# Performance work log

Measured on AMD Instinct MI355X. Metric: run time of the kernel, lower is better.

Reference implementation:

```python
import jax, jax.numpy as jnp
import numpy as np

EMBED_DIM = 1024
NUM_HEADS = 8
HEAD_DIM = EMBED_DIM // NUM_HEADS
SEQ_LEN = 128              # T: leaf sequence length of the tree
NODE_LEN = 2 * SEQ_LEN - 1 # Tk: nodes of a binary tree over T leaves
BATCH = 4
TGT_LEN = 128


def _tree_spans(lo, hi, out):
    # spans (lo, hi) of a balanced binary constituency tree, lo <= hi
    out.append((lo, hi))
    if lo == hi:
        return
    mid = (lo + hi) // 2
    _tree_spans(lo, mid, out)
    _tree_spans(mid + 1, hi, out)


def setup_inputs() -> dict:
    key = jax.random.key(0)
    ks = jax.random.split(key, 6)
    query = jax.random.normal(ks[0], (TGT_LEN, BATCH, EMBED_DIM), jnp.float32)
    key_t = jax.random.normal(ks[1], (NODE_LEN, BATCH, EMBED_DIM), jnp.float32)
    value = jax.random.normal(ks[2], (NODE_LEN, BATCH, EMBED_DIM), jnp.float32)
    spans = []
    _tree_spans(0, SEQ_LEN - 1, spans)
    spans = np.asarray(spans, dtype=np.int64)            # [Tk, 2], row <= col
    indices = jnp.asarray(np.broadcast_to(spans[None], (BATCH, NODE_LEN, 2)).copy())
    s = 1.0 / np.sqrt(EMBED_DIM)  # xavier-ish scale
    in_proj_weight = jax.random.uniform(ks[3], (3 * EMBED_DIM, EMBED_DIM), jnp.float32, -s, s)
    in_proj_bias = jnp.zeros((3 * EMBED_DIM,), jnp.float32)
    out_proj_weight = jax.random.uniform(ks[4], (EMBED_DIM, EMBED_DIM), jnp.float32, -s, s)
    out_proj_bias = jnp.zeros((EMBED_DIM,), jnp.float32)
    return {"query": query, "key": key_t, "value": value, "indices": indices,
            "in_proj_weight": in_proj_weight, "in_proj_bias": in_proj_bias,
            "out_proj_weight": out_proj_weight, "out_proj_bias": out_proj_bias}


def _forward(query, key, value, indices, in_proj_weight, in_proj_bias,
             out_proj_weight, out_proj_bias):
    T, H, D = SEQ_LEN, NUM_HEADS, HEAD_DIM
    lq, B, E = query.shape
    Tk = key.shape[0]
    wq, wk, wv = jnp.split(in_proj_weight, 3, axis=0)
    bq, bk, bv = jnp.split(in_proj_bias, 3)
    q = (query @ wq.T + bq) * (D ** -0.5)   # scaling = head_dim ** -0.5
    k = key @ wk.T + bk
    v = value @ wv.T + bv

    def to_heads(x):  # [L, B, E] -> [B*H, L, D]
        L = x.shape[0]
        return x.reshape(L, B * H, D).transpose(1, 0, 2)

    q, k, v = to_heads(q), to_heads(k), to_heads(v)

    # indices2flat_indices: fl_idx = row * T + col  -> [B, Tk]
    fl_idx = indices[:, :, 0] * T + indices[:, :, 1]

    # seq2matrix: scatter node keys into [B, H, D, T*T] span matrix
    k_b = k.reshape(B, H, Tk, D)

    def scat(kb, fb):  # kb [H, Tk, D], fb [Tk]
        return jnp.zeros((H, D, T * T), kb.dtype).at[:, :, fb].set(kb.transpose(0, 2, 1))

    mat_k = jax.vmap(scat)(k_b, fl_idx).reshape(B * H, D, T, T)

    # query2matrix + dot product: affinity[b,q,r,c] = <q_bq, k_node(r,c)> * triu(r<=c)
    triu = jnp.triu(jnp.ones((T, T), q.dtype))
    aff = jnp.einsum('bqd,bdrc->bqrc', q, mat_k) * triu  # [B*H, lq, T, T]

    # DP (hierarchical) accumulation over contained spans:
    # acc[r,c] = sum_{r <= r' <= c' <= c} aff[r',c']
    acc = jnp.flip(jnp.cumsum(jnp.flip(aff, axis=2), axis=2), axis=2)
    acc = jnp.cumsum(acc, axis=3)

    # gather scores back at node span positions -> [B, H, lq, Tk]
    acc = acc.reshape(B, H, lq, T * T)
    scores = jnp.take_along_axis(acc, fl_idx[:, None, None, :], axis=3)

    w = jax.nn.softmax(scores.reshape(B * H, lq, Tk), axis=-1)
    attn = jnp.einsum('bqn,bnd->bqd', w, v)              # [B*H, lq, D]
    attn = attn.transpose(1, 0, 2).reshape(lq, B, E)
    return attn @ out_proj_weight.T + out_proj_bias


def reference(query, key, value, indices, in_proj_weight, in_proj_bias,
              out_proj_weight, out_proj_bias):
    return _forward(query, key, value, indices, in_proj_weight, in_proj_bias,
                    out_proj_weight, out_proj_bias)
```

## Files before the change

### kernel.cpp

```cpp
#include <hip/hip_runtime.h>
#include <math.h>

#define EMBED 1024
#define NHEAD 8
#define HDIM 128
#define TK 255
#define BATCH 4
#define LQ 128
#define BH 32

typedef __attribute__((ext_vector_type(4))) float f32x4;
typedef __attribute__((ext_vector_type(8))) short short8;
typedef __attribute__((ext_vector_type(4))) short short4v;

static __device__ __forceinline__ unsigned short f2bf(float f) {
    unsigned u = __float_as_uint(f);
    u += 0x7FFFu + ((u >> 16) & 1u);
    return (unsigned short)(u >> 16);
}
static __device__ __forceinline__ float bfbits2f(unsigned short s) {
    return __uint_as_float(((unsigned)s) << 16);
}

__global__ __launch_bounds__(256) void prep_kernel(
    const float* __restrict__ query, const float* __restrict__ key_t,
    const float* __restrict__ value, const float* __restrict__ ipw,
    const float* __restrict__ opw,
    unsigned short* __restrict__ apk, unsigned short* __restrict__ wpk)
{
    const int blk = blockIdx.x;
    const int t = threadIdx.x;
    if (blk < 128) {
        const int b = blk >> 5, eg = blk & 31;
        const int cl = t & 31, seg = t >> 5;
        const int e = eg * 32 + cl;
        __shared__ float tot[8][33];
        float vals[32];
        float acc = 0.f;
        const int nhi = seg * 32 + 31;
        #pragma unroll
        for (int i = 0; i < 32; ++i) {
            const int n = nhi - i;
            float v = 0.f;
            if (n < TK) v = key_t[(long)(n * 4 + b) * 1024 + e];
            acc += v;
            vals[i] = acc;
        }
        tot[seg][cl] = acc;
        __syncthreads();
        float add = 0.f;
        #pragma unroll
        for (int s = 0; s < 8; ++s) if (s > seg) add += tot[s][cl];
        #pragma unroll
        for (int i = 0; i < 32; ++i) {
            const int n = nhi - i;
            const float f = vals[i] + add;
            const unsigned short hv = f2bf(f);
            const unsigned short lv = f2bf(f - bfbits2f(hv));
            unsigned short* dst = apk + (long)(512 + b * 256 + n) * 2048 + e;
            dst[0] = hv;
            dst[1024] = lv;
        }
    } else {
        const int APKC = 1536 * 256;
        const int TOT = APKC + 4096 * 256;
        for (int idx = (blk - 128) * 256 + t; idx < TOT; idx += 2048 * 256) {
            const bool isA = idx < APKC;
            const int rel = isA ? idx : idx - APKC;
            const int row = rel >> 8, c4 = rel & 255;
            const float* src = nullptr; long srow = 0;
            unsigned short* dst;
            bool wlo = true;
            if (isA) {
                if (row < 512) { src = query; srow = row; dst = apk + (long)row * 2048; }
                else {
                    const int vr = row - 512;
                    dst = apk + (long)(1536 + vr) * 2048;
                    if (vr < 1020) { src = value; srow = vr; }
                }
            } else {
                dst = wpk + (long)row * 2048;
                if (row < 3072) { src = ipw; srow = row; }
                else { src = opw; srow = row - 3072; }
                wlo = (row < 2048);
            }
            float4 f = make_float4(0.f, 0.f, 0.f, 0.f);
            if (src) f = *(const float4*)(src + srow * 1024 + c4 * 4);
            const unsigned short h0 = f2bf(f.x), h1 = f2bf(f.y), h2 = f2bf(f.z), h3 = f2bf(f.w);
            short4v hv;
            hv[0] = (short)h0; hv[1] = (short)h1; hv[2] = (short)h2; hv[3] = (short)h3;
            *(short4v*)(dst + c4 * 4) = hv;
            if (wlo) {
                short4v lv;
                lv[0] = (short)f2bf(f.x - bfbits2f(h0));
                lv[1] = (short)f2bf(f.y - bfbits2f(h1));
                lv[2] = (short)f2bf(f.z - bfbits2f(h2));
                lv[3] = (short)f2bf(f.w - bfbits2f(h3));
                *(short4v*)(dst + 1024 + c4 * 4) = lv;
            }
        }
    }
}

template<int BM, int BN, int TERMS, int EPI>
__device__ __forceinline__ void bgemm2(
    const unsigned short* __restrict__ A,
    const unsigned short* __restrict__ B,
    const float* __restrict__ bias,
    void* __restrict__ Cv, long ldc, float scale,
    int m0, int n0, unsigned char* lds)
{
    constexpr int AH = 0;
    constexpr int AL = BM * 128;
    constexpr int BHo = 2 * BM * 128;
    constexpr int BLo = BHo + BN * 128;
    constexpr int FM2 = BM / 32, FN2 = BN / 32;
    constexpr int CA = BM / 32;
    constexpr int CB = BN / 32;
    const int t = threadIdx.x, lane = t & 63, wave = t >> 6;
    const int wm = wave >> 1, wn = wave & 1;

    f32x4 acc[FM2][FN2];
    #pragma unroll
    for (int i = 0; i < FM2; ++i)
        #pragma unroll
        for (int j = 0; j < FN2; ++j)
            #pragma unroll
            for (int e = 0; e < 4; ++e) acc[i][j][e] = 0.f;

    const int srow_a = t >> 3, su = t & 7;
    short8 rah[CA], ral[CA], rbh[CB], rbl[CB];

    #pragma unroll
    for (int c = 0; c < CA; ++c) {
        const long base = (long)(m0 + c * 32 + srow_a) * 2048 + su * 8;
        rah[c] = *(const short8*)(A + base);
        ral[c] = *(const short8*)(A + base + 1024);
    }
    #pragma unroll
    for (int c = 0; c < CB; ++c) {
        const long base = (long)(n0 + c * 32 + srow_a) * 2048 + su * 8;
        rbh[c] = *(const short8*)(B + base);
        if (TERMS == 3) rbl[c] = *(const short8*)(B + base + 1024);
    }

    for (int kt = 0; kt < 16; ++kt) {
        #pragma unroll
        for (int c = 0; c < CA; ++c) {
            const int row = c * 32 + srow_a;
            const int byte = row * 128 + ((su ^ (row & 7)) << 4);
            *(short8*)(lds + AH + byte) = rah[c];
            *(short8*)(lds + AL + byte) = ral[c];
        }
        #pragma unroll
        for (int c = 0; c < CB; ++c) {
            const int row = c * 32 + srow_a;
            const int byte = row * 128 + ((su ^ (row & 7)) << 4);
            *(short8*)(lds + BHo + byte) = rbh[c];
            if (TERMS == 3) *(short8*)(lds + BLo + byte) = rbl[c];
        }
        __syncthreads();
        if (kt + 1 < 16) {
            const int off = (kt + 1) * 64;
            #pragma unroll
            for (int c = 0; c < CA; ++c) {
                const long base = (long)(m0 + c * 32 + srow_a) * 2048 + off + su * 8;
                rah[c] = *(const short8*)(A + base);
                ral[c] = *(const short8*)(A + base + 1024);
            }
            #pragma unroll
            for (int c = 0; c < CB; ++c) {
                const long base = (long)(n0 + c * 32 + srow_a) * 2048 + off + su * 8;
                rbh[c] = *(const short8*)(B + base);
                if (TERMS == 3) rbl[c] = *(const short8*)(B + base + 1024);
            }
        }
        #pragma unroll
        for (int ks = 0; ks < 2; ++ks) {
            short8 afh[FM2], afl[FM2], bgh[FN2], bgl[FN2];
            #pragma unroll
            for (int fm = 0; fm < FM2; ++fm) {
                const int row = wm * (BM / 2) + fm * 16 + (lane & 15);
                const int byte = row * 128 + (((ks * 4 + (lane >> 4)) ^ (row & 7)) << 4);
                afh[fm] = *(const short8*)(lds + AH + byte);
                afl[fm] = *(const short8*)(lds + AL + byte);
            }
            #pragma unroll
            for (int fn = 0; fn < FN2; ++fn) {
                const int row = wn * (BN / 2) + fn * 16 + (lane & 15);
                const int byte = row * 128 + (((ks * 4 + (lane >> 4)) ^ (row & 7)) << 4);
                bgh[fn] = *(const short8*)(lds + BHo + byte);
                if (TERMS == 3) bgl[fn] = *(const short8*)(lds + BLo + byte);
            }
            #pragma unroll
            for (int fm = 0; fm < FM2; ++fm)
                #pragma unroll
                for (int fn = 0; fn < FN2; ++fn) {
                    acc[fm][fn] = __builtin_amdgcn_mfma_f32_16x16x32_bf16(afh[fm], bgh[fn], acc[fm][fn], 0, 0, 0);
                    acc[fm][fn] = __builtin_amdgcn_mfma_f32_16x16x32_bf16(afl[fm], bgh[fn], acc[fm][fn], 0, 0, 0);
                    if (TERMS == 3)
                        acc[fm][fn] = __builtin_amdgcn_mfma_f32_16x16x32_bf16(afh[fm], bgl[fn], acc[fm][fn], 0, 0, 0);
                }
        }
        __syncthreads();
    }

    #pragma unroll
    for (int fm = 0; fm < FM2; ++fm)
        #pragma unroll
        for (int i = 0; i < 4; ++i) {
            const int m = m0 + wm * (BM / 2) + fm * 16 + ((lane >> 4) << 2) + i;
            #pragma unroll
            for (int fn = 0; fn < FN2; ++fn) {
                const int n = n0 + wn * (BN / 2) + fn * 16 + (lane & 15);
                float v = acc[fm][fn][i];
                if (EPI == 0) {
                    float* C = (float*)Cv;
                    if (bias) v += bias[n];
                    C[(long)m * ldc + n] = v * scale;
                } else if (EPI == 1) {
                    float* C = (float*)Cv;
                    v += (float)(255 - (m & 255)) * bias[n];
                    C[(long)m * ldc + n] = v;
                } else if (EPI == 2) {
                    unsigned short* C = (unsigned short*)Cv;
                    const float val = (v + bias[n]) * scale;
                    const unsigned short hv = f2bf(val);
                    const unsigned short lv = f2bf(val - bfbits2f(hv));
                    C[(long)m * 2048 + n] = hv;
                    C[(long)m * 2048 + 1024 + n] = lv;
                } else {
                    unsigned short* C = (unsigned short*)Cv;
                    const float val = v + bias[n];
                    C[(long)m * 1024 + n] = f2bf(val);
                }
            }
        }
}

__global__ __launch_bounds__(256) void qkvb_kernel(
    const unsigned short* __restrict__ apk, const unsigned short* __restrict__ wpk,
    const float* __restrict__ ipb,
    unsigned short* __restrict__ qpk, float* __restrict__ sbuf,
    unsigned short* __restrict__ vpk, float qscale)
{
    __shared__ __align__(16) unsigned char lds[4 * 64 * 128];
    const int lid = blockIdx.y * 16 + blockIdx.x;
    const int xcd = lid & 7, slot = lid >> 3;
    const int y = xcd * 5 + (slot >> 4);
    const int x = slot & 15;
    if (y < 8) {
        bgemm2<64, 64, 3, 2>(apk, wpk, ipb, qpk, 2048, qscale,
                             y * 64, x * 64, lds);
    } else if (y < 24) {
        bgemm2<64, 64, 3, 1>(apk + 512L * 2048, wpk + 1024L * 2048, ipb + 1024, sbuf, 1024, 1.f,
                             (y - 8) * 64, x * 64, lds);
    } else {
        bgemm2<64, 64, 2, 3>(apk + 1536L * 2048, wpk + 2048L * 2048, ipb + 2048, vpk, 1024, 1.f,
                             (y - 24) * 64, x * 64, lds);
    }
}

__global__ __launch_bounds__(256) void outprojb_kernel(
    const unsigned short* __restrict__ apk2, const unsigned short* __restrict__ wpk,
    const float* __restrict__ opb, float* __restrict__ out)
{
    __shared__ __align__(16) unsigned char lds[(2 * 32 + 64) * 128];
    const int lid = blockIdx.x;
    const int xcd = lid & 7, slot = lid >> 3;
    const int y = xcd * 2 + (slot >> 4);
    const int x = slot & 15;
    bgemm2<32, 64, 2, 0>(apk2, wpk + 3072L * 2048, opb, out, 1024, 1.f,
                         y * 32, x * 64, lds);
}

#define F_QH 0
#define F_QL 8192
#define F_KH 16384
#define F_KL 32768
#define F_PH 49152
#define F_RED 65536
#define F_INV 66048

__global__ __launch_bounds__(256, 2) void fused_attn_kernel(
    const unsigned short* __restrict__ qpk, const float* __restrict__ sbuf,
    const unsigned short* __restrict__ vpk, const int* __restrict__ indices,
    unsigned short* __restrict__ apk2)
{
    __shared__ __align__(16) unsigned char lds[66176];
    __shared__ int onode[256];
    const int lid = blockIdx.x;
    const int xcd = lid & 7, slot = lid >> 3;
    const int bh = xcd * 4 + (slot >> 2), qq = slot & 3;
    const int b = bh >> 3, h = bh & 7;
    const int t = threadIdx.x, lane = t & 63, wave = t >> 6;
    const int wm = wave >> 1, wn = wave & 1;
    float* red = (float*)(lds + F_RED);
    float* inv = (float*)(lds + F_INV);

    if (t < TK) {
        const int r0 = indices[(b * TK + t) * 2 + 0];
        const int c0 = indices[(b * TK + t) * 2 + 1];
        onode[t] = t + 2 * (c0 - r0) + 1;
    } else if (t < 256) {
        onode[t] = 255;
    }

    {
        #pragma unroll
        for (int rr = 0; rr < 4; ++rr) {
            const int chunk = rr * 256 + t;
            const int row = chunk >> 5;
            const int rem = chunk & 31;
            const int plane = rem >> 4, u = rem & 15;
            const int tq = qq * 32 + row;
            short8 v = *(const short8*)(qpk + (long)(tq * 4 + b) * 2048 + plane * 1024 + h * 128 + u * 8);
            const int byte = row * 256 + ((u ^ (row & 15)) << 4);
            *(short8*)(lds + (plane ? F_QL : F_QH) + byte) = v;
        }
    }

    f32x4 acc[4][2];
    #pragma unroll
    for (int nb = 0; nb < 4; ++nb)
        #pragma unroll
        for (int j = 0; j < 2; ++j)
            #pragma unroll
            for (int e = 0; e < 4; ++e) acc[nb][j][e] = 0.f;

    #pragma unroll
    for (int nb = 0; nb < 4; ++nb) {
        __syncthreads();
        {
            const int c4 = t & 31, r8 = t >> 5;
            const float* sb = sbuf + (long)b * 256 * 1024 + h * 128 + c4 * 4;
            #pragma unroll
            for (int rr = 0; rr < 8; ++rr) {
                const int nl = r8 + rr * 8;
                const int node = nb * 64 + nl;
                float4 f0 = *(const float4*)(sb + (long)node * 1024);
                float4 f1 = *(const float4*)(sb + (long)onode[node] * 1024);
                float4 f = make_float4(f0.x - f1.x, f0.y - f1.y, f0.z - f1.z, f0.w - f1.w);
                const unsigned short h0 = f2bf(f.x), h1 = f2bf(f.y), h2 = f2bf(f.z), h3 = f2bf(f.w);
                short4v hv, lv;
                hv[0] = (short)h0; hv[1] = (short)h1; hv[2] = (short)h2; hv[3] = (short)h3;
                lv[0] = (short)f2bf(f.x - bfbits2f(h0));
                lv[1] = (short)f2bf(f.y - bfbits2f(h1));
                lv[2] = (short)f2bf(f.z - bfbits2f(h2));
                lv[3] = (short)f2bf(f.w - bfbits2f(h3));
                const int byte = nl * 256 + ((((c4 >> 1) ^ (nl & 15)) << 4) | ((c4 & 1) << 3));
                *(short4v*)(lds + F_KH + byte) = hv;
                *(short4v*)(lds + F_KL + byte) = lv;
            }
        }
        __syncthreads();
        #pragma unroll
        for (int ks = 0; ks < 4; ++ks) {
            short8 ah, al, bh_[2], bl[2];
            {
                const int row = wm * 16 + (lane & 15);
                const int byte = row * 256 + (((ks * 4 + (lane >> 4)) ^ (row & 15)) << 4);
                ah = *(const short8*)(lds + F_QH + byte);
                al = *(const short8*)(lds + F_QL + byte);
            }
            #pragma unroll
            for (int fn = 0; fn < 2; ++fn) {
                const int row = wn * 32 + fn * 16 + (lane & 15);
                const int byte = row * 256 + (((ks * 4 + (lane >> 4)) ^ (row & 15)) << 4);
                bh_[fn] = *(const short8*)(lds + F_KH + byte);
                bl[fn] = *(const short8*)(lds + F_KL + byte);
            }
            #pragma unroll
            for (int fn = 0; fn < 2; ++fn) {
                acc[nb][fn] = __builtin_amdgcn_mfma_f32_16x16x32_bf16(ah, bh_[fn], acc[nb][fn], 0, 0, 0);
                acc[nb][fn] = __builtin_amdgcn_mfma_f32_16x16x32_bf16(al, bh_[fn], acc[nb][fn], 0, 0, 0);
                acc[nb][fn] = __builtin_amdgcn_mfma_f32_16x16x32_bf16(ah, bl[fn], acc[nb][fn], 0, 0, 0);
            }
        }
    }

    float pmax[4] = {-1e30f, -1e30f, -1e30f, -1e30f};
    #pragma unroll
    for (int nb = 0; nb < 4; ++nb)
        #pragma unroll
        for (int fn = 0; fn < 2; ++fn)
            #pragma unroll
            for (int i = 0; i < 4; ++i) {
                const int col = nb * 64 + wn * 32 + fn * 16 + (lane & 15);
                const float s = (col < TK) ? acc[nb][fn][i] : -1e30f;
                pmax[i] = fmaxf(pmax[i], s);
            }
    #pragma unroll
    for (int off = 1; off < 16; off <<= 1)
        #pragma unroll
        for (int i = 0; i < 4; ++i) pmax[i] = fmaxf(pmax[i], __shfl_xor(pmax[i], off));
    if ((lane & 15) == 0) {
        #pragma unroll
        for (int i = 0; i < 4; ++i) {
            const int row = wm * 16 + ((lane >> 4) << 2) + i;
            red[wn * 32 + row] = pmax[i];
        }
    }
    __syncthreads();
    float rm[4];
    #pragma unroll
    for (int i = 0; i < 4; ++i) {
        const int row = wm * 16 + ((lane >> 4) << 2) + i;
        rm[i] = fmaxf(red[row], red[32 + row]);
    }
    float psum[4] = {0.f, 0.f, 0.f, 0.f};
    #pragma unroll
    for (int nb = 0; nb < 4; ++nb)
        #pragma unroll
        for (int fn = 0; fn < 2; ++fn)
            #pragma unroll
            for (int i = 0; i < 4; ++i) {
                const int col = nb * 64 + wn * 32 + fn * 16 + (lane & 15);
                const int row = wm * 16 + ((lane >> 4) << 2) + i;
                float p = 0.f;
                if (col < TK) p = __expf(acc[nb][fn][i] - rm[i]);
                psum[i] += p;
                const unsigned short hp = f2bf(p);
                const int u = ((col >> 3) ^ ((row & 15) << 1));
                const int byte = row * 512 + (u << 4) + (col & 7) * 2;
                *(unsigned short*)(lds + F_PH + byte) = hp;
            }
    #pragma unroll
    for (int off = 1; off < 16; off <<= 1)
        #pragma unroll
        for (int i = 0; i < 4; ++i) psum[i] += __shfl_xor(psum[i], off);
    if ((lane & 15) == 0) {
        #pragma unroll
        for (int i = 0; i < 4; ++i) {
            const int row = wm * 16 + ((lane >> 4) << 2) + i;
            red[64 + wn * 32 + row] = psum[i];
        }
    }
    __syncthreads();
    if (wn == 0 && (lane & 15) == 0) {
        #pragma unroll
        for (int i = 0; i < 4; ++i) {
            const int row = wm * 16 + ((lane >> 4) << 2) + i;
            inv[row] = 1.f / (red[64 + row] + red[96 + row]);
        }
    }

    f32x4 accO[4];
    #pragma unroll
    for (int fn = 0; fn < 4; ++fn)
        #pragma unroll
        for (int e = 0; e < 4; ++e) accO[fn][e] = 0.f;

    #pragma unroll
    for (int nb = 0; nb < 4; ++nb) {
        __syncthreads();
        {
            const int c8 = t & 15, r16 = t >> 4;
            #pragma unroll
            for (int rr = 0; rr < 4; ++rr) {
                const int nl = r16 + rr * 16;
                const int node = nb * 64 + nl;
                short8 v = {0, 0, 0, 0, 0, 0, 0, 0};
                if (node < TK) v = *(const short8*)(vpk + (long)(node * 4 + b) * 1024 + h * 128 + c8 * 8);
                #pragma unroll
                for (int j = 0; j < 8; ++j) {
                    const int d = c8 * 8 + j;
                    const int byte = d * 128 + ((((nl >> 3) ^ (d & 7)) << 4) | ((nl & 7) << 1));
                    *(unsigned short*)(lds + F_KH + byte) = (unsigned short)v[j];
                }
            }
        }
        __syncthreads();
        #pragma unroll
        for (int ks = 0; ks < 2; ++ks) {
            short8 pa, vb[4];
            {
                const int row = wm * 16 + (lane & 15);
                const int u = (nb * 8 + ks * 4 + (lane >> 4)) ^ ((row & 15) << 1);
                const int byte = row * 512 + (u << 4);
                pa = *(const short8*)(lds + F_PH + byte);
            }
            #pragma unroll
            for (int fn = 0; fn < 4; ++fn) {
                const int d = wn * 64 + fn * 16 + (lane & 15);
                const int u = (ks * 4 + (lane >> 4)) ^ (d & 7);
                const int byte = d * 128 + (u << 4);
                vb[fn] = *(const short8*)(lds + F_KH + byte);
            }
            #pragma unroll
            for (int fn = 0; fn < 4; ++fn)
                accO[fn] = __builtin_amdgcn_mfma_f32_16x16x32_bf16(pa, vb[fn], accO[fn], 0, 0, 0);
        }
    }

    __syncthreads();
    #pragma unroll
    for (int i = 0; i < 4; ++i) {
        const int row = wm * 16 + ((lane >> 4) << 2) + i;
        const float iv = inv[row];
        const int arow = (qq * 32 + row) * 4 + b;
        #pragma unroll
        for (int fn = 0; fn < 4; ++fn) {
            const int col = h * 128 + wn * 64 + fn * 16 + (lane & 15);
            const float val = accO[fn][i] * iv;
            const unsigned short hv = f2bf(val);
            const unsigned short lv = f2bf(val - bfbits2f(hv));
            apk2[(long)arow * 2048 + col] = hv;
            apk2[(long)arow * 2048 + 1024 + col] = lv;
        }
    }
}

extern "C" void kernel_launch(void* const* d_in, const int* in_sizes, int n_in,
                              void* d_out, int out_size, void* d_ws, size_t ws_size,
                              hipStream_t stream) {
    const float* query   = (const float*)d_in[0];
    const float* key_t   = (const float*)d_in[1];
    const float* value   = (const float*)d_in[2];
    const int*   indices = (const int*)d_in[3];
    const float* ipw     = (const float*)d_in[4];
    const float* ipb     = (const float*)d_in[5];
    const float* opw     = (const float*)d_in[6];
    const float* opb     = (const float*)d_in[7];
    float* out = (float*)d_out;

    float* ws = (float*)d_ws;
    float* sbuf = ws;
    unsigned short* qpk = (unsigned short*)(sbuf + 1048576);
    unsigned short* vpk = qpk + 512L * 2048;
    unsigned short* apk = vpk + 1024L * 1024;
    unsigned short* wpk = apk + 2560L * 2048;
    unsigned short* apk2 = apk;

    const float qscale = 0.08838834764831843f;

    prep_kernel<<<dim3(2176), 256, 0, stream>>>(query, key_t, value, ipw, opw, apk, wpk);

    qkvb_kernel<<<dim3(16, 40), 256, 0, stream>>>(apk, wpk, ipb, qpk, sbuf, vpk, qscale);

    fused_attn_kernel<<<dim3(128), 256, 0, stream>>>(qpk, sbuf, vpk, indices, apk2);

    outprojb_kernel<<<dim3(256), 256, 0, stream>>>(apk2, wpk, opb, out);
}
```

Baseline: 70.19 us.

## Split fused attention into 16-row query tiles to double block count

The fused attention kernel now handles 16 query rows per block instead of 32 and launches 256 blocks instead of 128, so more CUs on the MI355X are used. The four waves now split the key/value columns only, not rows, and the cross-wave max/sum reductions combine four partials. LDS use drops to about 49 KB. The price is that every block redoes the K-difference staging and bf16 split and the V transpose from global memory, so that staging work doubles overall.

Measured after the change: 69.54 us, median of 2. About the same (-0.9%).

```diff
diff --git a/kernel.cpp b/kernel.cpp
--- a/kernel.cpp
+++ b/kernel.cpp
@@ -275,26 +275,25 @@
 }
 
 #define F_QH 0
-#define F_QL 8192
-#define F_KH 16384
-#define F_KL 32768
-#define F_PH 49152
-#define F_RED 65536
-#define F_INV 66048
+#define F_QL 4096
+#define F_KH 8192
+#define F_KL 24576
+#define F_PH 40960
+#define F_RED 49152
+#define F_INV 49664
 
 __global__ __launch_bounds__(256, 2) void fused_attn_kernel(
     const unsigned short* __restrict__ qpk, const float* __restrict__ sbuf,
     const unsigned short* __restrict__ vpk, const int* __restrict__ indices,
     unsigned short* __restrict__ apk2)
 {
-    __shared__ __align__(16) unsigned char lds[66176];
+    __shared__ __align__(16) unsigned char lds[49728];
     __shared__ int onode[256];
     const int lid = blockIdx.x;
     const int xcd = lid & 7, slot = lid >> 3;
-    const int bh = xcd * 4 + (slot >> 2), qq = slot & 3;
+    const int bh = xcd * 4 + (slot >> 3), qq8 = slot & 7;
     const int b = bh >> 3, h = bh & 7;
-    const int t = threadIdx.x, lane = t & 63, wave = t >> 6;
-    const int wm = wave >> 1, wn = wave & 1;
+    const int t = threadIdx.x, lane = t & 63, wn = t >> 6;
     float* red = (float*)(lds + F_RED);
     float* inv = (float*)(lds + F_INV);
 
@@ -308,25 +307,23 @@
 
     {
         #pragma unroll
-        for (int rr = 0; rr < 4; ++rr) {
+        for (int rr = 0; rr < 2; ++rr) {
             const int chunk = rr * 256 + t;
             const int row = chunk >> 5;
             const int rem = chunk & 31;
             const int plane = rem >> 4, u = rem & 15;
-            const int tq = qq * 32 + row;
+            const int tq = qq8 * 16 + row;
             short8 v = *(const short8*)(qpk + (long)(tq * 4 + b) * 2048 + plane * 1024 + h * 128 + u * 8);
             const int byte = row * 256 + ((u ^ (row & 15)) << 4);
             *(short8*)(lds + (plane ? F_QL : F_QH) + byte) = v;
         }
     }
 
-    f32x4 acc[4][2];
+    f32x4 acc[4];
     #pragma unroll
     for (int nb = 0; nb < 4; ++nb)
         #pragma unroll
-        for (int j = 0; j < 2; ++j)
-            #pragma unroll
-            for (int e = 0; e < 4; ++e) acc[nb][j][e] = 0.f;
+        for (int e = 0; e < 4; ++e) acc[nb][e] = 0.f;
 
     #pragma unroll
     for (int nb = 0; nb < 4; ++nb) {
@@ -356,26 +353,22 @@
         __syncthreads();
         #pragma unroll
         for (int ks = 0; ks < 4; ++ks) {
-            short8 ah, al, bh_[2], bl[2];
+            short8 ah, al, bh_, bl;
             {
-                const int row = wm * 16 + (lane & 15);
+                const int row = lane & 15;
                 const int byte = row * 256 + (((ks * 4 + (lane >> 4)) ^ (row & 15)) << 4);
                 ah = *(const short8*)(lds + F_QH + byte);
                 al = *(const short8*)(lds + F_QL + byte);
             }
-            #pragma unroll
-            for (int fn = 0; fn < 2; ++fn) {
-                const int row = wn * 32 + fn * 16 + (lane & 15);
-                const int byte = row * 256 + (((ks * 4 + (lane >> 4)) ^ (row & 15)) << 4);
-                bh_[fn] = *(const short8*)(lds + F_KH + byte);
-                bl[fn] = *(const short8*)(lds + F_KL + byte);
-            }
-            #pragma unroll
-            for (int fn = 0; fn < 2; ++fn) {
-                acc[nb][fn] = __builtin_amdgcn_mfma_f32_16x16x32_bf16(ah, bh_[fn], acc[nb][fn], 0, 0, 0);
-                acc[nb][fn] = __builtin_amdgcn_mfma_f32_16x16x32_bf16(al, bh_[fn], acc[nb][fn], 0, 0, 0);
-                acc[nb][fn] = __builtin_amdgcn_mfma_f32_16x16x32_bf16(ah, bl[fn], acc[nb][fn], 0, 0, 0);
-            }
+            {
+                const int rown = wn * 16 + (lane & 15);
+                const int byte = rown * 256 + (((ks * 4 + (lane >> 4)) ^ (rown & 15)) << 4);
+                bh_ = *(const short8*)(lds + F_KH + byte);
+                bl = *(const short8*)(lds + F_KL + byte);
+            }
+            acc[nb] = __builtin_amdgcn_mfma_f32_16x16x32_bf16(ah, bh_, acc[nb], 0, 0, 0);
+            acc[nb] = __builtin_amdgcn_mfma_f32_16x16x32_bf16(al, bh_, acc[nb], 0, 0, 0);
+            acc[nb] = __builtin_amdgcn_mfma_f32_16x16x32_bf16(ah, bl, acc[nb], 0, 0, 0);
         }
     }
 
@@ -383,13 +376,11 @@
     #pragma unroll
     for (int nb = 0; nb < 4; ++nb)
         #pragma unroll
-        for (int fn = 0; fn < 2; ++fn)
-            #pragma unroll
-            for (int i = 0; i < 4; ++i) {
-                const int col = nb * 64 + wn * 32 + fn * 16 + (lane & 15);
-                const float s = (col < TK) ? acc[nb][fn][i] : -1e30f;
-                pmax[i] = fmaxf(pmax[i], s);
-            }
+        for (int i = 0; i < 4; ++i) {
+            const int col = nb * 64 + wn * 16 + (lane & 15);
+            const float s = (col < TK) ? acc[nb][i] : -1e30f;
+            pmax[i] = fmaxf(pmax[i], s);
+        }
     #pragma unroll
     for (int off = 1; off < 16; off <<= 1)
         #pragma unroll
@@ -397,34 +388,32 @@
     if ((lane & 15) == 0) {
         #pragma unroll
         for (int i = 0; i < 4; ++i) {
-            const int row = wm * 16 + ((lane >> 4) << 2) + i;
-            red[wn * 32 + row] = pmax[i];
+            const int row = ((lane >> 4) << 2) + i;
+            red[wn * 16 + row] = pmax[i];
         }
     }
     __syncthreads();
     float rm[4];
     #pragma unroll
     for (int i = 0; i < 4; ++i) {
-        const int row = wm * 16 + ((lane >> 4) << 2) + i;
-        rm[i] = fmaxf(red[row], red[32 + row]);
+        const int row = ((lane >> 4) << 2) + i;
+        rm[i] = fmaxf(fmaxf(red[row], red[16 + row]), fmaxf(red[32 + row], red[48 + row]));
     }
     float psum[4] = {0.f, 0.f, 0.f, 0.f};
     #pragma unroll
     for (int nb = 0; nb < 4; ++nb)
         #pragma unroll
-        for (int fn = 0; fn < 2; ++fn)
-            #pragma unroll
-            for (int i = 0; i < 4; ++i) {
-                const int col = nb * 64 + wn * 32 + fn * 16 + (lane & 15);
-                const int row = wm * 16 + ((lane >> 4) << 2) + i;
-                float p = 0.f;
-                if (col < TK) p = __expf(acc[nb][fn][i] - rm[i]);
-                psum[i] += p;
-                const unsigned short hp = f2bf(p);
-                const int u = ((col >> 3) ^ ((row & 15) << 1));
-                const int byte = row * 512 + (u << 4) + (col & 7) * 2;
-                *(unsigned short*)(lds + F_PH + byte) = hp;
-            }
+        for (int i = 0; i < 4; ++i) {
+            const int col = nb * 64 + wn * 16 + (lane & 15);
+            const int row = ((lane >> 4) << 2) + i;
+            float p = 0.f;
+            if (col < TK) p = __expf(acc[nb][i] - rm[i]);
+            psum[i] += p;
+            const unsigned short hp = f2bf(p);
+            const int u = ((col >> 3) ^ ((row & 15) << 1));
+            const int byte = row * 512 + (u << 4) + (col & 7) * 2;
+            *(unsigned short*)(lds + F_PH + byte) = hp;
+        }
     #pragma unroll
     for (int off = 1; off < 16; off <<= 1)
         #pragma unroll
@@ -432,22 +421,22 @@
     if ((lane & 15) == 0) {
         #pragma unroll
         for (int i = 0; i < 4; ++i) {
-            const int row = wm * 16 + ((lane >> 4) << 2) + i;
-            red[64 + wn * 32 + row] = psum[i];
+            const int row = ((lane >> 4) << 2) + i;
+            red[64 + wn * 16 + row] = psum[i];
         }
     }
     __syncthreads();
     if (wn == 0 && (lane & 15) == 0) {
         #pragma unroll
         for (int i = 0; i < 4; ++i) {
-            const int row = wm * 16 + ((lane >> 4) << 2) + i;
-            inv[row] = 1.f / (red[64 + row] + red[96 + row]);
-        }
-    }
-
-    f32x4 accO[4];
-    #pragma unroll
-    for (int fn = 0; fn < 4; ++fn)
+            const int row = ((lane >> 4) << 2) + i;
+            inv[row] = 1.f / (red[64 + row] + red[80 + row] + red[96 + row] + red[112 + row]);
+        }
+    }
+
+    f32x4 accO[2];
+    #pragma unroll
+    for (int fn = 0; fn < 2; ++fn)
         #pragma unroll
         for (int e = 0; e < 4; ++e) accO[fn][e] = 0.f;
 
@@ -473,22 +462,22 @@
         __syncthreads();
         #pragma unroll
         for (int ks = 0; ks < 2; ++ks) {
-            short8 pa, vb[4];
+            short8 pa, vb[2];
             {
-                const int row = wm * 16 + (lane & 15);
+                const int row = lane & 15;
                 const int u = (nb * 8 + ks * 4 + (lane >> 4)) ^ ((row & 15) << 1);
                 const int byte = row * 512 + (u << 4);
                 pa = *(const short8*)(lds + F_PH + byte);
             }
             #pragma unroll
-            for (int fn = 0; fn < 4; ++fn) {
-                const int d = wn * 64 + fn * 16 + (lane & 15);
+            for (int fn = 0; fn < 2; ++fn) {
+                const int d = wn * 32 + fn * 16 + (lane & 15);
                 const int u = (ks * 4 + (lane >> 4)) ^ (d & 7);
                 const int byte = d * 128 + (u << 4);
                 vb[fn] = *(const short8*)(lds + F_KH + byte);
             }
             #pragma unroll
-            for (int fn = 0; fn < 4; ++fn)
+            for (int fn = 0; fn < 2; ++fn)
                 accO[fn] = __builtin_amdgcn_mfma_f32_16x16x32_bf16(pa, vb[fn], accO[fn], 0, 0, 0);
         }
     }
@@ -496,12 +485,12 @@
     __syncthreads();
     #pragma unroll
     for (int i = 0; i < 4; ++i) {
-        const int row = wm * 16 + ((lane >> 4) << 2) + i;
+        const int row = ((lane >> 4) << 2) + i;
         const float iv = inv[row];
-        const int arow = (qq * 32 + row) * 4 + b;
-        #pragma unroll
-        for (int fn = 0; fn < 4; ++fn) {
-            const int col = h * 128 + wn * 64 + fn * 16 + (lane & 15);
+        const int arow = (qq8 * 16 + row) * 4 + b;
+        #pragma unroll
+        for (int fn = 0; fn < 2; ++fn) {
+            const int col = h * 128 + wn * 32 + fn * 16 + (lane & 15);
             const float val = accO[fn][i] * iv;
             const unsigned short hv = f2bf(val);
             const unsigned short lv = f2bf(val - bfbits2f(hv));
@@ -538,7 +527,7 @@
 
     qkvb_kernel<<<dim3(16, 40), 256, 0, stream>>>(apk, wpk, ipb, qpk, sbuf, vpk, qscale);
 
-    fused_attn_kernel<<<dim3(128), 256, 0, stream>>>(qpk, sbuf, vpk, indices, apk2);
+    fused_attn_kernel<<<dim3(256), 256, 0, stream>>>(qpk, sbuf, vpk, indices, apk2);
 
     outprojb_kernel<<<dim3(256), 256, 0, stream>>>(apk2, wpk, opb, out);
 }
```
